# Performance work log

Measured on AMD Instinct MI355X. Metric: run time of the kernel, lower is better.

## Reference

```python
import jax, jax.numpy as jnp
import numpy as np


def setup_inputs() -> dict:
    key = jax.random.key(0)
    k1, k2, k3, k4 = jax.random.split(key, 4)
    B, S, E = 4, 2048, 2048
    x = jax.random.normal(k1, (B, S, E), dtype=jnp.float32)
    w_query = jax.random.normal(k2, (E, E), dtype=jnp.float32)
    w_key = jax.random.normal(k3, (E, E), dtype=jnp.float32)
    w_value = jax.random.normal(k4, (E, E), dtype=jnp.float32)
    return {"x": x, "w_query": w_query, "w_key": w_key, "w_value": w_value}


def reference(x, w_query, w_key, w_value):
    B, S, E = x.shape
    H = 16
    Dh = E // H  # query_size
    scale = 1.0 / jnp.sqrt(jnp.float32(Dh))
    # NOTE: original uses reshape (NOT transpose) from (B,S,H,Dh) -> (B,H,S,Dh),
    # a pure reinterpretation of the flat buffer. Replicate with direct reshape.
    q = (x @ w_query).reshape(B, H, S, Dh)
    k = (x @ w_key).reshape(B, H, S, Dh)
    v = (x @ w_value).reshape(B, H, S, Dh)
    scores = jnp.einsum("bhqd,bhkd->bhqk", q, k) * scale
    # original applies Softmax(dim=0) to each (S,S) score matrix -> query axis
    soft = jax.nn.softmax(scores, axis=2)
    attn = jnp.einsum("bhqk,bhkd->bhqd", soft, v)  # (B,H,S,Dh)
    # original: reshape (B,H,S,Dh)->(B,S,H,Dh)->(B,S,E), both pure reshapes
    return attn.reshape(B, S, E)
```

## Files before the change

kernel.cpp:

```cpp
#include <hip/hip_runtime.h>
#include <math.h>

typedef _Float16 half_t;
typedef __attribute__((ext_vector_type(8))) _Float16 f16x8;
typedef __attribute__((ext_vector_type(4))) _Float16 f16x4;
typedef __attribute__((ext_vector_type(4))) float f32x4;

#define MFMA __builtin_amdgcn_mfma_f32_16x16x32_f16
#define K1C (0.08838834764831845f * 1.4426950408889634f)
#define RLO (1.0f / 2048.0f)

__device__ inline void gld16(const void* g, void* l) {
  __builtin_amdgcn_global_load_lds(
      (const __attribute__((address_space(1))) uint32_t*)g,
      (__attribute__((address_space(3))) uint32_t*)l, 16, 0, 0);
}

__global__ __launch_bounds__(256) void split_x(const float* __restrict__ X,
                                               half_t* __restrict__ Xh,
                                               half_t* __restrict__ Xl) {
  size_t i = (size_t)blockIdx.x * 256 + threadIdx.x;
  const size_t stride = (size_t)gridDim.x * 256;
  for (size_t p = i; p < 4194304; p += stride) {
    f32x4 v = ((const f32x4*)X)[p];
    f16x4 h, l;
#pragma unroll
    for (int j = 0; j < 4; ++j) {
      half_t hh = (half_t)v[j];
      h[j] = hh;
      l[j] = (half_t)((v[j] - (float)hh) * 2048.0f);
    }
    ((f16x4*)Xh)[p] = h;
    ((f16x4*)Xl)[p] = l;
  }
}

__global__ __launch_bounds__(256) void wtrans_split(const float* __restrict__ W,
                                                    half_t* __restrict__ Wh,
                                                    half_t* __restrict__ Wl) {
  __shared__ float T[64][68];
  const int tid = threadIdx.x;
  const int k0 = blockIdx.x * 64, n0 = blockIdx.y * 64;
#pragma unroll
  for (int t = 0; t < 4; ++t) {
    int s = t * 256 + tid;
    int kr = s >> 4, nc = (s & 15) * 4;
    f32x4 v = *(const f32x4*)&W[(size_t)(k0 + kr) * 2048 + n0 + nc];
#pragma unroll
    for (int j = 0; j < 4; ++j) T[nc + j][kr] = v[j];
  }
  __syncthreads();
#pragma unroll
  for (int t = 0; t < 4; ++t) {
    int s = t * 256 + tid;
    int nr = s >> 4, kc = (s & 15) * 4;
    f16x4 h, l;
#pragma unroll
    for (int j = 0; j < 4; ++j) {
      float q = T[nr][kc + j];
      half_t hh = (half_t)q;
      h[j] = hh;
      l[j] = (half_t)((q - (float)hh) * 2048.0f);
    }
    *(f16x4*)&Wh[(size_t)(n0 + nr) * 2048 + k0 + kc] = h;
    *(f16x4*)&Wl[(size_t)(n0 + nr) * 2048 + k0 + kc] = l;
  }
}

#define STAGE_P(nb, kn) do {                                                  \
    _Pragma("unroll")                                                         \
    for (int t_ = 0; t_ < 2; ++t_) {                                          \
      int s_ = t_ * 256 + tid;                                                \
      int row_ = s_ >> 2;                                                     \
      int lch_ = (s_ & 3) ^ ((row_ >> 1) & 3);       \
      size_t ga_ = (size_t)(m0 + row_) * 2048 + (kn) + lch_ * 8;              \
      size_t gb_ = (size_t)(n0 + row_) * 2048 + (kn) + lch_ * 8;              \
      gld16(&Xh[ga_], &sAh[nb][s_ * 8]);                                      \
      gld16(&Xl[ga_], &sAl[nb][s_ * 8]);                                      \
      gld16(&Wh[gb_], &sBh[nb][s_ * 8]);                                      \
      gld16(&Wl[gb_], &sBl[nb][s_ * 8]);                                      \
    }                                                                         \
  } while (0)

__global__ __launch_bounds__(256, 2) void proj_mfma(
    const half_t* __restrict__ Xh, const half_t* __restrict__ Xl,
    const half_t* __restrict__ Wh, const half_t* __restrict__ Wl,
    half_t* __restrict__ Ch, half_t* __restrict__ Cl, const int mode) {
  __shared__ half_t sAh[2][4096], sAl[2][4096], sBh[2][4096], sBl[2][4096];
  const int tid = threadIdx.x;
  const int lid = blockIdx.x;
  const int swz = (lid & 7) * 128 + (lid >> 3);
  const int m0 = (swz >> 4) << 7, n0 = (swz & 15) << 7;
  const int w = tid >> 6, lane = tid & 63, c = lane & 15, g = lane >> 4;
  const int wr = w >> 1, wc = w & 1;
  f32x4 z4 = {0.f, 0.f, 0.f, 0.f};
  f32x4 acc0[4][4], accX[4][4];
#pragma unroll
  for (int i = 0; i < 4; ++i)
#pragma unroll
    for (int j = 0; j < 4; ++j) { acc0[i][j] = z4; accX[i][j] = z4; }
  STAGE_P(0, 0);
  __syncthreads();
  for (int k0 = 0; k0 < 2048; k0 += 32) {
    const int buf = (k0 >> 5) & 1;
    if (k0 < 2016) STAGE_P(buf ^ 1, k0 + 32);
    {
      f16x8 a0[4], a1[4], b0[4], b1[4];
      const int sw = g ^ ((c >> 1) & 3);
#pragma unroll
      for (int i = 0; i < 4; ++i) {
        int ar = wr * 64 + i * 16 + c;
        a0[i] = *(const f16x8*)&sAh[buf][ar * 32 + sw * 8];
        a1[i] = *(const f16x8*)&sAl[buf][ar * 32 + sw * 8];
        int br = wc * 64 + i * 16 + c;
        b0[i] = *(const f16x8*)&sBh[buf][br * 32 + sw * 8];
        b1[i] = *(const f16x8*)&sBl[buf][br * 32 + sw * 8];
      }
#pragma unroll
      for (int i = 0; i < 4; ++i)
#pragma unroll
        for (int j = 0; j < 4; ++j) {
          acc0[i][j] = MFMA(a0[i], b0[j], acc0[i][j], 0, 0, 0);
          if (mode == 0) {
            accX[i][j] = MFMA(a0[i], b1[j], accX[i][j], 0, 0, 0);
            accX[i][j] = MFMA(a1[i], b0[j], accX[i][j], 0, 0, 0);
          }
        }
    }
    __syncthreads();
  }
#pragma unroll
  for (int i = 0; i < 4; ++i)
#pragma unroll
    for (int j = 0; j < 4; ++j) {
      int mbase = m0 + wr * 64 + i * 16 + g * 4;
      int n = n0 + wc * 64 + j * 16 + c;
#pragma unroll
      for (int r = 0; r < 4; ++r) {
        float q = acc0[i][j][r] + accX[i][j][r] * RLO;
        half_t hh = (half_t)q;
        size_t o = (size_t)(mbase + r) * 2048 + n;
        Ch[o] = hh;
        if (mode == 0) Cl[o] = (half_t)((q - (float)hh) * 2048.0f);
      }
    }
}

__global__ __launch_bounds__(256) void transpose_v(const half_t* __restrict__ V,
                                                   half_t* __restrict__ Vt) {
  __shared__ half_t T[128 * 128];
  const int tid = threadIdx.x;
  const int bh = blockIdx.y, k0 = blockIdx.x * 128;
  const size_t base = (size_t)bh << 18;
#pragma unroll
  for (int t = 0; t < 8; ++t) {
    int s = t * 256 + tid;
    int kr = s >> 4, ch = s & 15;
    int pc = ch ^ ((kr >> 3) & 15);
    *(f16x8*)&T[kr * 128 + pc * 8] =
        *(const f16x8*)&V[base + (size_t)(k0 + kr) * 128 + ch * 8];
  }
  __syncthreads();
#pragma unroll
  for (int t = 0; t < 8; ++t) {
    int s = t * 256 + tid;
    int d = s >> 4, kc = s & 15;
    f16x8 o;
#pragma unroll
    for (int j = 0; j < 8; ++j) {
      int kr = kc * 8 + j;
      int pc = (d >> 3) ^ (kc & 15);
      o[j] = T[kr * 128 + pc * 8 + (d & 7)];
    }
    *(f16x8*)&Vt[base + (size_t)d * 2048 + k0 + kc * 8] = o;
  }
}

#define STAGE_Q(nb, qn) do {                                                  \
    int r0_ = tid >> 4, cl0_ = tid & 15;                                      \
    size_t o0_ = base + (size_t)((qn) + r0_) * 128 + ((cl0_ ^ r0_) << 3);     \
    gld16(&Qh[o0_], &sQ0[nb][tid << 3]);                                      \
    gld16(&Ql[o0_], &sQ1[nb][tid << 3]);                                      \
    int r1_ = 16 + r0_;                                                       \
    size_t o1_ = base + (size_t)((qn) + r1_) * 128 + ((cl0_ ^ (r1_ & 15)) << 3); \
    gld16(&Qh[o1_], &sQ0[nb][(256 + tid) << 3]);                              \
    gld16(&Ql[o1_], &sQ1[nb][(256 + tid) << 3]);                              \
  } while (0)

__global__ __launch_bounds__(256, 2) void stats_mfma(
    const half_t* __restrict__ Qh, const half_t* __restrict__ Ql,
    const half_t* __restrict__ Kh, const half_t* __restrict__ Kl,
    float* __restrict__ C2) {
  __shared__ half_t sQ0[2][4096], sQ1[2][4096];
  const int tid = threadIdx.x;
  const int w = tid >> 6, lane = tid & 63, c = lane & 15, g = lane >> 4;
  const int lid = blockIdx.y * 8 + blockIdx.x;
  const int bh = (lid & 7) * 8 + ((lid >> 3) & 7);
  const int xb = lid >> 6;
  const size_t base = (size_t)bh << 18;
  const int kb = xb * 256 + w * 64;
  f32x4 z4 = {0.f, 0.f, 0.f, 0.f};
  f16x8 ka0[4][4], ka1[4][4];
#pragma unroll
  for (int kt = 0; kt < 4; ++kt)
#pragma unroll
    for (int ds = 0; ds < 4; ++ds) {
      size_t a = base + (size_t)(kb + kt * 16 + c) * 128 + ds * 32 + g * 8;
      ka0[kt][ds] = *(const f16x8*)&Kh[a];
      ka1[kt][ds] = *(const f16x8*)&Kl[a];
    }
  float m[4][4], z[4][4];
#pragma unroll
  for (int kt = 0; kt < 4; ++kt)
#pragma unroll
    for (int r = 0; r < 4; ++r) { m[kt][r] = -INFINITY; z[kt][r] = 0.f; }
  STAGE_Q(0, 0);
  __syncthreads();
  for (int t = 0; t < 64; ++t) {
    const int buf = t & 1;
    if (t < 63) STAGE_Q(buf ^ 1, (t + 1) << 5);
#pragma unroll
    for (int qh = 0; qh < 2; ++qh) {
      f16x8 q0v[4], q1v[4];
#pragma unroll
      for (int ds = 0; ds < 4; ++ds) {
        int off = ((qh << 4) | c) * 128 + ((((ds << 2) | g) ^ c) << 3);
        q0v[ds] = *(const f16x8*)&sQ0[buf][off];
        q1v[ds] = *(const f16x8*)&sQ1[buf][off];
      }
#pragma unroll
      for (int kt = 0; kt < 4; ++kt) {
        f32x4 A0 = z4, AX = z4;
#pragma unroll
        for (int ds = 0; ds < 4; ++ds) {
          A0 = MFMA(ka0[kt][ds], q0v[ds], A0, 0, 0, 0);
          AX = MFMA(ka0[kt][ds], q1v[ds], AX, 0, 0, 0);
          AX = MFMA(ka1[kt][ds], q0v[ds], AX, 0, 0, 0);
        }
#pragma unroll
        for (int r = 0; r < 4; ++r) {
          float tt = (A0[r] + AX[r] * RLO) * K1C;
          float mo = m[kt][r];
          float mn = fmaxf(mo, tt);
          float e = __builtin_amdgcn_exp2f(fminf(mo, tt) - mn);
          z[kt][r] = (tt <= mo) ? (z[kt][r] + e) : (z[kt][r] * e + 1.0f);
          m[kt][r] = mn;
        }
      }
    }
    __syncthreads();
  }
#pragma unroll
  for (int mask = 1; mask < 16; mask <<= 1)
#pragma unroll
    for (int kt = 0; kt < 4; ++kt)
#pragma unroll
      for (int r = 0; r < 4; ++r) {
        float mo = __shfl_xor(m[kt][r], mask, 64);
        float zo = __shfl_xor(z[kt][r], mask, 64);
        float mn = fmaxf(m[kt][r], mo);
        z[kt][r] = z[kt][r] * __builtin_amdgcn_exp2f(m[kt][r] - mn) +
                   zo * __builtin_amdgcn_exp2f(mo - mn);
        m[kt][r] = mn;
      }
  if (c == 0) {
#pragma unroll
    for (int kt = 0; kt < 4; ++kt)
#pragma unroll
      for (int r = 0; r < 4; ++r)
        C2[(bh << 11) + kb + kt * 16 + (g << 2) + r] =
            m[kt][r] + __builtin_amdgcn_logf(z[kt][r]);
  }
}

#define STAGE_ATTN(nb, ktn) do {                                              \
    int r_ = tid >> 4, chl_ = tid & 15;                                       \
    size_t ro_ = base + (size_t)((ktn) + r_) * 128 + ((chl_ ^ (r_ & 15)) << 3); \
    gld16(&Kh[ro_], &sKh[nb][tid << 3]);                                      \
    gld16(&Kl[ro_], &sKl[nb][tid << 3]);                                      \
    int d_ = tid >> 2, cvl_ = tid & 3;                                        \
    gld16(&Vt[base + (size_t)d_ * 2048 + (ktn) + ((cvl_ ^ ((d_ >> 1) & 3)) << 3)], \
          &sVs[nb][tid << 3]);                                                \
  } while (0)

__global__ __launch_bounds__(512, 4) void attn_mfma(
    const half_t* __restrict__ Qh, const half_t* __restrict__ Ql,
    const half_t* __restrict__ Kh, const half_t* __restrict__ Kl,
    const half_t* __restrict__ Vt, const float* __restrict__ C2,
    float* __restrict__ O) {
  __shared__ half_t sKh[2][4096], sKl[2][4096], sVs[2][4096];
  __shared__ half_t sP[8][16][40];
  __shared__ float sC2[2048];
  const int tid = threadIdx.x;
  const int w = tid >> 6, lane = tid & 63, c = lane & 15, g = lane >> 4;
  const int lid = blockIdx.y * 16 + blockIdx.x;
  const int bh = (lid & 7) * 8 + ((lid >> 3) & 7);
  const int qx = lid >> 6;
  const size_t base = (size_t)bh << 18;
  const int qb = qx * 128 + w * 16;
  f32x4 z4 = {0.f, 0.f, 0.f, 0.f};
  f16x8 qf0[4], qf1[4];
#pragma unroll
  for (int ds = 0; ds < 4; ++ds) {
    size_t a = base + (size_t)(qb + c) * 128 + ds * 32 + g * 8;
    qf0[ds] = *(const f16x8*)&Qh[a];
    qf1[ds] = *(const f16x8*)&Ql[a];
  }
  f32x4 Oacc[8];
#pragma unroll
  for (int dt = 0; dt < 8; ++dt) Oacc[dt] = z4;
  ((f32x4*)sC2)[tid] = ((const f32x4*)(C2 + ((size_t)bh << 11)))[tid];
  STAGE_ATTN(0, 0);
  __syncthreads();
  for (int t = 0; t < 64; ++t) {
    const int buf = t & 1;
    const int kt = t << 5;
    if (t < 63) STAGE_ATTN(buf ^ 1, kt + 32);
#pragma unroll
    for (int h = 0; h < 2; ++h) {
      f32x4 A0 = z4, AX = z4;
#pragma unroll
      for (int ds = 0; ds < 4; ++ds) {
        int off = ((h << 4) | c) * 128 + ((((ds << 2) | g) ^ c) << 3);
        f16x8 k0v = *(const f16x8*)&sKh[buf][off];
        f16x8 k1v = *(const f16x8*)&sKl[buf][off];
        A0 = MFMA(k0v, qf0[ds], A0, 0, 0, 0);
        AX = MFMA(k0v, qf1[ds], AX, 0, 0, 0);
        AX = MFMA(k1v, qf0[ds], AX, 0, 0, 0);
      }
      f32x4 c2v = *(const f32x4*)&sC2[kt + (h << 4) + (g << 2)];
      f16x4 pv;
#pragma unroll
      for (int r = 0; r < 4; ++r)
        pv[r] = (half_t)__builtin_amdgcn_exp2f((A0[r] + AX[r] * RLO) * K1C - c2v[r]);
      *(f16x4*)&sP[w][c][(h << 4) + (g << 2)] = pv;
    }
    f16x8 pa = *(const f16x8*)&sP[w][c][g << 3];
#pragma unroll
    for (int dt = 0; dt < 8; ++dt) {
      int dd = (dt << 4) + c;
      f16x8 vb = *(const f16x8*)&sVs[buf][dd * 32 + ((g ^ ((dd >> 1) & 3)) << 3)];
      Oacc[dt] = MFMA(pa, vb, Oacc[dt], 0, 0, 0);
    }
    __syncthreads();
  }
#pragma unroll
  for (int dt = 0; dt < 8; ++dt)
#pragma unroll
    for (int r = 0; r < 4; ++r)
      O[base + (size_t)(qb + (g << 2) + r) * 128 + (dt << 4) + c] = Oacc[dt][r];
}

extern "C" void kernel_launch(void* const* d_in, const int* in_sizes, int n_in,
                              void* d_out, int out_size, void* d_ws, size_t ws_size,
                              hipStream_t stream) {
  (void)in_sizes; (void)n_in; (void)out_size; (void)ws_size;
  const float* x = (const float*)d_in[0];
  const float* wq = (const float*)d_in[1];
  const float* wk = (const float*)d_in[2];
  const float* wv = (const float*)d_in[3];
  float* out = (float*)d_out;
  char* ws = (char*)d_ws;
  const size_t S2 = 33554432;
  half_t* Wth = (half_t*)ws;
  half_t* Wtl = (half_t*)(ws + 8388608);
  half_t* Qh = (half_t*)(ws + 16777216);
  half_t* Ql = (half_t*)(ws + 16777216 + S2);
  half_t* Kh = (half_t*)(ws + 16777216 + 2 * S2);
  half_t* Kl = (half_t*)(ws + 16777216 + 3 * S2);
  half_t* Vh = (half_t*)(ws + 16777216 + 4 * S2);
  half_t* Vth = (half_t*)(ws + 16777216 + 5 * S2);
  float* C2 = (float*)(ws + 16777216 + 6 * S2);
  half_t* Xh = (half_t*)d_out;
  half_t* Xl = (half_t*)((char*)d_out + S2);
  dim3 b(256);
  split_x<<<2048, b, 0, stream>>>(x, Xh, Xl);
  wtrans_split<<<dim3(32, 32), b, 0, stream>>>(wq, Wth, Wtl);
  proj_mfma<<<dim3(1024), b, 0, stream>>>(Xh, Xl, Wth, Wtl, Qh, Ql, 0);
  wtrans_split<<<dim3(32, 32), b, 0, stream>>>(wk, Wth, Wtl);
  proj_mfma<<<dim3(1024), b, 0, stream>>>(Xh, Xl, Wth, Wtl, Kh, Kl, 0);
  wtrans_split<<<dim3(32, 32), b, 0, stream>>>(wv, Wth, Wtl);
  proj_mfma<<<dim3(1024), b, 0, stream>>>(Xh, Xl, Wth, Wtl, Vh, nullptr, 1);
  transpose_v<<<dim3(16, 64), b, 0, stream>>>(Vh, Vth);
  stats_mfma<<<dim3(8, 64), b, 0, stream>>>(Qh, Ql, Kh, Kl, C2);
  attn_mfma<<<dim3(16, 64), dim3(512), 0, stream>>>(Qh, Ql, Kh, Kl, Vth, C2, out);
}
```

Baseline: 1.085 ms.

## Use 32x32 MFMA in projections, template mode, split stats over query chunks

The projection GEMM switches from 16x16x32 to 32x32x16 MFMA tiles, which cuts LDS fragment reads per FLOP, and is templated on mode. That removes the runtime branch, the unused low-part loads and the unused shared memory for the V projection, and raises its occupancy hint. The softmax statistics kernel is split four ways over the query axis so more blocks run in parallel. A new finalize kernel merges the partial max and sum values, at the cost of an extra launch and workspace traffic.

```diff
diff --git a/kernel.cpp b/kernel.cpp
--- a/kernel.cpp
+++ b/kernel.cpp
@@ -5,8 +5,10 @@
 typedef __attribute__((ext_vector_type(8))) _Float16 f16x8;
 typedef __attribute__((ext_vector_type(4))) _Float16 f16x4;
 typedef __attribute__((ext_vector_type(4))) float f32x4;
+typedef __attribute__((ext_vector_type(16))) float f32x16;
 
 #define MFMA __builtin_amdgcn_mfma_f32_16x16x32_f16
+#define MFMA32 __builtin_amdgcn_mfma_f32_32x32x16_f16
 #define K1C (0.08838834764831845f * 1.4426950408889634f)
 #define RLO (1.0f / 2048.0f)
 
@@ -75,73 +77,85 @@
       int lch_ = (s_ & 3) ^ ((row_ >> 1) & 3);       \
       size_t ga_ = (size_t)(m0 + row_) * 2048 + (kn) + lch_ * 8;              \
       size_t gb_ = (size_t)(n0 + row_) * 2048 + (kn) + lch_ * 8;              \
-      gld16(&Xh[ga_], &sAh[nb][s_ * 8]);                                      \
-      gld16(&Xl[ga_], &sAl[nb][s_ * 8]);                                      \
-      gld16(&Wh[gb_], &sBh[nb][s_ * 8]);                                      \
-      gld16(&Wl[gb_], &sBl[nb][s_ * 8]);                                      \
+      gld16(&Xh[ga_], &sm[nb][s_ * 8]);                                       \
+      gld16(&Wh[gb_], &sm[nb][4096 + s_ * 8]);                                \
+      if constexpr (MODE == 0) {                                              \
+        gld16(&Xl[ga_], &sm[nb][8192 + s_ * 8]);                              \
+        gld16(&Wl[gb_], &sm[nb][12288 + s_ * 8]);                             \
+      }                                                                       \
     }                                                                         \
   } while (0)
 
-__global__ __launch_bounds__(256, 2) void proj_mfma(
+template <int MODE>
+__global__ __launch_bounds__(256, MODE == 0 ? 2 : 4) void proj_mfma(
     const half_t* __restrict__ Xh, const half_t* __restrict__ Xl,
     const half_t* __restrict__ Wh, const half_t* __restrict__ Wl,
-    half_t* __restrict__ Ch, half_t* __restrict__ Cl, const int mode) {
-  __shared__ half_t sAh[2][4096], sAl[2][4096], sBh[2][4096], sBl[2][4096];
+    half_t* __restrict__ Ch, half_t* __restrict__ Cl) {
+  __shared__ half_t sm[2][MODE == 0 ? 16384 : 8192];
   const int tid = threadIdx.x;
   const int lid = blockIdx.x;
   const int swz = (lid & 7) * 128 + (lid >> 3);
   const int m0 = (swz >> 4) << 7, n0 = (swz & 15) << 7;
-  const int w = tid >> 6, lane = tid & 63, c = lane & 15, g = lane >> 4;
+  const int w = tid >> 6, lane = tid & 63, r5 = lane & 31, hi = lane >> 5;
   const int wr = w >> 1, wc = w & 1;
-  f32x4 z4 = {0.f, 0.f, 0.f, 0.f};
-  f32x4 acc0[4][4], accX[4][4];
-#pragma unroll
-  for (int i = 0; i < 4; ++i)
-#pragma unroll
-    for (int j = 0; j < 4; ++j) { acc0[i][j] = z4; accX[i][j] = z4; }
+  const int rsw = (r5 >> 1) & 3;
+  f32x16 acc0[2][2], accX[2][2];
+#pragma unroll
+  for (int i = 0; i < 2; ++i)
+#pragma unroll
+    for (int j = 0; j < 2; ++j) {
+#pragma unroll
+      for (int r = 0; r < 16; ++r) { acc0[i][j][r] = 0.f; accX[i][j][r] = 0.f; }
+    }
   STAGE_P(0, 0);
   __syncthreads();
   for (int k0 = 0; k0 < 2048; k0 += 32) {
     const int buf = (k0 >> 5) & 1;
     if (k0 < 2016) STAGE_P(buf ^ 1, k0 + 32);
-    {
-      f16x8 a0[4], a1[4], b0[4], b1[4];
-      const int sw = g ^ ((c >> 1) & 3);
-#pragma unroll
-      for (int i = 0; i < 4; ++i) {
-        int ar = wr * 64 + i * 16 + c;
-        a0[i] = *(const f16x8*)&sAh[buf][ar * 32 + sw * 8];
-        a1[i] = *(const f16x8*)&sAl[buf][ar * 32 + sw * 8];
-        int br = wc * 64 + i * 16 + c;
-        b0[i] = *(const f16x8*)&sBh[buf][br * 32 + sw * 8];
-        b1[i] = *(const f16x8*)&sBl[buf][br * 32 + sw * 8];
-      }
-#pragma unroll
-      for (int i = 0; i < 4; ++i)
-#pragma unroll
-        for (int j = 0; j < 4; ++j) {
-          acc0[i][j] = MFMA(a0[i], b0[j], acc0[i][j], 0, 0, 0);
-          if (mode == 0) {
-            accX[i][j] = MFMA(a0[i], b1[j], accX[i][j], 0, 0, 0);
-            accX[i][j] = MFMA(a1[i], b0[j], accX[i][j], 0, 0, 0);
+#pragma unroll
+    for (int ks = 0; ks < 2; ++ks) {
+      const int ch = ((ks << 1) | hi) ^ rsw;
+      f16x8 a0[2], a1[2], b0[2], b1[2];
+#pragma unroll
+      for (int i = 0; i < 2; ++i) {
+        int ar = wr * 64 + i * 32 + r5;
+        int br = wc * 64 + i * 32 + r5;
+        a0[i] = *(const f16x8*)&sm[buf][ar * 32 + ch * 8];
+        b0[i] = *(const f16x8*)&sm[buf][4096 + br * 32 + ch * 8];
+        if constexpr (MODE == 0) {
+          a1[i] = *(const f16x8*)&sm[buf][8192 + ar * 32 + ch * 8];
+          b1[i] = *(const f16x8*)&sm[buf][12288 + br * 32 + ch * 8];
+        }
+      }
+#pragma unroll
+      for (int i = 0; i < 2; ++i)
+#pragma unroll
+        for (int j = 0; j < 2; ++j) {
+          acc0[i][j] = MFMA32(a0[i], b0[j], acc0[i][j], 0, 0, 0);
+          if constexpr (MODE == 0) {
+            accX[i][j] = MFMA32(a0[i], b1[j], accX[i][j], 0, 0, 0);
+            accX[i][j] = MFMA32(a1[i], b0[j], accX[i][j], 0, 0, 0);
           }
         }
     }
     __syncthreads();
   }
 #pragma unroll
-  for (int i = 0; i < 4; ++i)
-#pragma unroll
-    for (int j = 0; j < 4; ++j) {
-      int mbase = m0 + wr * 64 + i * 16 + g * 4;
-      int n = n0 + wc * 64 + j * 16 + c;
-#pragma unroll
-      for (int r = 0; r < 4; ++r) {
-        float q = acc0[i][j][r] + accX[i][j][r] * RLO;
+  for (int i = 0; i < 2; ++i)
+#pragma unroll
+    for (int j = 0; j < 2; ++j) {
+      int mb = m0 + wr * 64 + i * 32 + 4 * hi;
+      int n = n0 + wc * 64 + j * 32 + r5;
+#pragma unroll
+      for (int r = 0; r < 16; ++r) {
+        int mrow = mb + (r & 3) + 8 * (r >> 2);
+        float q;
+        if constexpr (MODE == 0) q = acc0[i][j][r] + accX[i][j][r] * RLO;
+        else q = acc0[i][j][r];
         half_t hh = (half_t)q;
-        size_t o = (size_t)(mbase + r) * 2048 + n;
+        size_t o = (size_t)mrow * 2048 + n;
         Ch[o] = hh;
-        if (mode == 0) Cl[o] = (half_t)((q - (float)hh) * 2048.0f);
+        if constexpr (MODE == 0) Cl[o] = (half_t)((q - (float)hh) * 2048.0f);
       }
     }
 }
@@ -190,13 +204,14 @@
 __global__ __launch_bounds__(256, 2) void stats_mfma(
     const half_t* __restrict__ Qh, const half_t* __restrict__ Ql,
     const half_t* __restrict__ Kh, const half_t* __restrict__ Kl,
-    float* __restrict__ C2) {
+    float* __restrict__ Mp, float* __restrict__ Zp) {
   __shared__ half_t sQ0[2][4096], sQ1[2][4096];
   const int tid = threadIdx.x;
   const int w = tid >> 6, lane = tid & 63, c = lane & 15, g = lane >> 4;
   const int lid = blockIdx.y * 8 + blockIdx.x;
   const int bh = (lid & 7) * 8 + ((lid >> 3) & 7);
   const int xb = lid >> 6;
+  const int qstart = blockIdx.z << 9;
   const size_t base = (size_t)bh << 18;
   const int kb = xb * 256 + w * 64;
   f32x4 z4 = {0.f, 0.f, 0.f, 0.f};
@@ -214,11 +229,11 @@
   for (int kt = 0; kt < 4; ++kt)
 #pragma unroll
     for (int r = 0; r < 4; ++r) { m[kt][r] = -INFINITY; z[kt][r] = 0.f; }
-  STAGE_Q(0, 0);
+  STAGE_Q(0, qstart);
   __syncthreads();
-  for (int t = 0; t < 64; ++t) {
+  for (int t = 0; t < 16; ++t) {
     const int buf = t & 1;
-    if (t < 63) STAGE_Q(buf ^ 1, (t + 1) << 5);
+    if (t < 15) STAGE_Q(buf ^ 1, qstart + ((t + 1) << 5));
 #pragma unroll
     for (int qh = 0; qh < 2; ++qh) {
       f16x8 q0v[4], q1v[4];
@@ -264,13 +279,31 @@
         m[kt][r] = mn;
       }
   if (c == 0) {
+    const int pb = (blockIdx.z << 17) + (bh << 11);
 #pragma unroll
     for (int kt = 0; kt < 4; ++kt)
 #pragma unroll
-      for (int r = 0; r < 4; ++r)
-        C2[(bh << 11) + kb + kt * 16 + (g << 2) + r] =
-            m[kt][r] + __builtin_amdgcn_logf(z[kt][r]);
-  }
+      for (int r = 0; r < 4; ++r) {
+        int idx = pb + kb + kt * 16 + (g << 2) + r;
+        Mp[idx] = m[kt][r];
+        Zp[idx] = z[kt][r];
+      }
+  }
+}
+
+__global__ __launch_bounds__(256) void stats_finalize(const float* __restrict__ Mp,
+                                                      const float* __restrict__ Zp,
+                                                      float* __restrict__ C2) {
+  int i = blockIdx.x * 256 + threadIdx.x;
+  float m = Mp[i], z = Zp[i];
+#pragma unroll
+  for (int s = 1; s < 4; ++s) {
+    float ms = Mp[(s << 17) + i], zs = Zp[(s << 17) + i];
+    float mn = fmaxf(m, ms);
+    z = z * __builtin_amdgcn_exp2f(m - mn) + zs * __builtin_amdgcn_exp2f(ms - mn);
+    m = mn;
+  }
+  C2[i] = m + __builtin_amdgcn_logf(z);
 }
 
 #define STAGE_ATTN(nb, ktn) do {                                              \
@@ -371,17 +404,20 @@
   half_t* Vh = (half_t*)(ws + 16777216 + 4 * S2);
   half_t* Vth = (half_t*)(ws + 16777216 + 5 * S2);
   float* C2 = (float*)(ws + 16777216 + 6 * S2);
+  float* Mp = C2 + 131072;
+  float* Zp = Mp + 524288;
   half_t* Xh = (half_t*)d_out;
   half_t* Xl = (half_t*)((char*)d_out + S2);
   dim3 b(256);
   split_x<<<2048, b, 0, stream>>>(x, Xh, Xl);
   wtrans_split<<<dim3(32, 32), b, 0, stream>>>(wq, Wth, Wtl);
-  proj_mfma<<<dim3(1024), b, 0, stream>>>(Xh, Xl, Wth, Wtl, Qh, Ql, 0);
+  proj_mfma<0><<<dim3(1024), b, 0, stream>>>(Xh, Xl, Wth, Wtl, Qh, Ql);
   wtrans_split<<<dim3(32, 32), b, 0, stream>>>(wk, Wth, Wtl);
-  proj_mfma<<<dim3(1024), b, 0, stream>>>(Xh, Xl, Wth, Wtl, Kh, Kl, 0);
+  proj_mfma<0><<<dim3(1024), b, 0, stream>>>(Xh, Xl, Wth, Wtl, Kh, Kl);
   wtrans_split<<<dim3(32, 32), b, 0, stream>>>(wv, Wth, Wtl);
-  proj_mfma<<<dim3(1024), b, 0, stream>>>(Xh, Xl, Wth, Wtl, Vh, nullptr, 1);
+  proj_mfma<1><<<dim3(1024), b, 0, stream>>>(Xh, Xl, Wth, Wtl, Vh, nullptr);
   transpose_v<<<dim3(16, 64), b, 0, stream>>>(Vh, Vth);
-  stats_mfma<<<dim3(8, 64), b, 0, stream>>>(Qh, Ql, Kh, Kl, C2);
+  stats_mfma<<<dim3(8, 64, 4), b, 0, stream>>>(Qh, Ql, Kh, Kl, Mp, Zp);
+  stats_finalize<<<dim3(512), b, 0, stream>>>(Mp, Zp, C2);
   attn_mfma<<<dim3(16, 64), dim3(512), 0, stream>>>(Qh, Ql, Kh, Kl, Vth, C2, out);
 }
```

New measurement: 1.076 ms, median of 2. Within noise of the previous version (-0.9%).
